# Kernel tuning notes

Hardware: AMD Instinct MI355X
Metric: run time of the kernel (lower is better)

## Reference

```python
import jax, jax.numpy as jnp
import numpy as np

N = 100000   # nodes
E = 1600000  # edges (before self-loops)
F = 128      # num_features
H = 128      # hidden_dim
EPS = 1e-5   # BatchNorm eps


def setup_inputs() -> dict:
    key = jax.random.key(0)
    ks = jax.random.split(key, 8)
    x = jax.random.normal(ks[0], (N, F), dtype=jnp.float32)
    edge_index = jax.random.randint(ks[1], (2, E), 0, N, dtype=jnp.int64)

    def lin(k, din, dout):
        s = 1.0 / np.sqrt(din)
        kw, kb = jax.random.split(k)
        W = jax.random.uniform(kw, (din, dout), jnp.float32, -s, s)
        b = jax.random.uniform(kb, (dout,), jnp.float32, -s, s)
        return W, b

    W1, b1 = lin(ks[2], F, H)
    W2, b2 = lin(ks[3], H, H)
    W3, b3 = lin(ks[4], H, H)
    Wc, bc = lin(ks[5], H, 2)

    def bn_params():
        return (jnp.ones((H,), jnp.float32), jnp.zeros((H,), jnp.float32),
                jnp.zeros((H,), jnp.float32), jnp.ones((H,), jnp.float32))

    g1, be1, rm1, rv1 = bn_params()
    g2, be2, rm2, rv2 = bn_params()
    g3, be3, rm3, rv3 = bn_params()

    return {"x": x, "edge_index": edge_index,
            "W1": W1, "b1": b1, "W2": W2, "b2": b2, "W3": W3, "b3": b3,
            "g1": g1, "be1": be1, "rm1": rm1, "rv1": rv1,
            "g2": g2, "be2": be2, "rm2": rm2, "rv2": rv2,
            "g3": g3, "be3": be3, "rm3": rm3, "rv3": rv3,
            "Wc": Wc, "bc": bc}


def _gcn_norm(edge_index, num_nodes):
    # add self-loops, compute symmetric normalization (PyG GCNConv default)
    loop = jnp.arange(num_nodes, dtype=edge_index.dtype)
    src = jnp.concatenate([edge_index[0], loop])
    dst = jnp.concatenate([edge_index[1], loop])
    deg = jax.ops.segment_sum(jnp.ones_like(dst, dtype=jnp.float32), dst,
                              num_segments=num_nodes)
    dinv = jnp.where(deg > 0, jax.lax.rsqrt(deg), 0.0)
    norm = dinv[src] * dinv[dst]  # [E+N]
    return src, dst, norm


def _gcn_conv(x, W, b, src, dst, norm, num_nodes):
    h = x @ W                              # [N, H] linear first
    msg = h[src] * norm[:, None]           # gather + scale  [E+N, H]
    out = jax.ops.segment_sum(msg, dst, num_segments=num_nodes)  # scatter-add
    return out + b


def _bn_eval(x, g, be, rm, rv):
    return (x - rm) * jax.lax.rsqrt(rv + EPS) * g + be


def reference(x, edge_index,
              W1, b1, W2, b2, W3, b3,
              g1, be1, rm1, rv1,
              g2, be2, rm2, rv2,
              g3, be3, rm3, rv3,
              Wc, bc):
    n = x.shape[0]
    src, dst, norm = _gcn_norm(edge_index, n)
    h = _gcn_conv(x, W1, b1, src, dst, norm, n)
    h = _bn_eval(jax.nn.relu(h), g1, be1, rm1, rv1)
    # dropout: identity in eval mode
    h = _gcn_conv(h, W2, b2, src, dst, norm, n)
    h = _bn_eval(jax.nn.relu(h), g2, be2, rm2, rv2)
    h = _gcn_conv(h, W3, b3, src, dst, norm, n)
    h = _bn_eval(jax.nn.relu(h), g3, be3, rm3, rv3)
    return h @ Wc + bc  # [N, 2]
```

## Files before the change

### kernel.cpp

```cpp
#include <hip/hip_runtime.h>
#include <hip/hip_fp16.h>

#define BN_EPS 1e-5f
#define CHUNK 4096
#define BBITS 7

typedef _Float16 half8 __attribute__((ext_vector_type(8)));
typedef float f32x4 __attribute__((ext_vector_type(4)));

__device__ __forceinline__ float4 f4zero() { return make_float4(0.f, 0.f, 0.f, 0.f); }


__global__ __launch_bounds__(256) void k_pack_hist(const float* __restrict__ W1,
                                                   const float* __restrict__ W2,
                                                   const float* __restrict__ W3,
                                                   _Float16* __restrict__ pW,
                                                   const int* __restrict__ dst,
                                                   int* __restrict__ tableT,
                                                   int nA, int nbuck, int e) {
    __shared__ int h[1024];
    int tid = threadIdx.x;
    if (blockIdx.x < 24) {
        int t = blockIdx.x * 256 + tid;
        int wi = t >> 11;
        int tt = t & 2047;
        const float* W = (wi == 0) ? W1 : ((wi == 1) ? W2 : W3);
        int kc = tt >> 9;
        int rem = tt & 511;
        int ct = rem >> 6;
        int lane = rem & 63;
        int q = lane >> 4;
        int col = ct * 16 + (lane & 15);
        half8 hh;
#pragma unroll
        for (int j = 0; j < 8; ++j)
            hh[j] = (_Float16)W[(kc * 32 + q * 8 + j) * 128 + col];
        *(half8*)(pW + (size_t)t * 8) = hh;
        return;
    }
    int blk = blockIdx.x - 24;
    for (int k = tid; k < 1024; k += 256) h[k] = 0;
    __syncthreads();
    int base = blk * CHUNK;
    if (base + CHUNK <= e && (e & 3) == 0) {
        const int4* d4 = (const int4*)(dst + base);
#pragma unroll
        for (int t = 0; t < CHUNK / 1024; ++t) {
            int4 d = d4[t * 256 + tid];
            atomicAdd(&h[d.x >> BBITS], 1);
            atomicAdd(&h[d.y >> BBITS], 1);
            atomicAdd(&h[d.z >> BBITS], 1);
            atomicAdd(&h[d.w >> BBITS], 1);
        }
    } else {
        for (int i = base + tid; i < e && i < base + CHUNK; i += 256)
            atomicAdd(&h[dst[i] >> BBITS], 1);
    }
    __syncthreads();
    for (int k = tid; k < nbuck; k += 256)
        tableT[(size_t)k * nA + blk] = h[k];
}


__global__ __launch_bounds__(1024) void k_scan_block(const int* __restrict__ in,
                                                     int* __restrict__ outp,
                                                     int* __restrict__ partials, int len) {
    __shared__ int s[1024];
    int t = threadIdx.x;
    int gid = blockIdx.x * 1024 + t;
    int v = (gid < len) ? in[gid] : 0;
    int x = v;
    s[t] = x;
    __syncthreads();
    for (int d = 1; d < 1024; d <<= 1) {
        int y = (t >= d) ? s[t - d] : 0;
        __syncthreads();
        x += y;
        s[t] = x;
        __syncthreads();
    }
    if (gid < len) outp[gid] = x - v;
    if (t == 1023) partials[blockIdx.x] = x;
}

__global__ __launch_bounds__(256) void k_scan_addp(int* __restrict__ data,
                                                   const int* __restrict__ partials, int len) {
    __shared__ int red[256];
    int tid = threadIdx.x;
    int K = blockIdx.x >> 2;
    int s = 0;
    for (int t = tid; t < K; t += 256) s += partials[t];
    red[tid] = s;
    __syncthreads();
    for (int d = 128; d > 0; d >>= 1) {
        if (tid < d) red[tid] += red[tid + d];
        __syncthreads();
    }
    int gid = blockIdx.x * 256 + tid;
    if (gid < len) data[gid] += red[0];
}


template <bool AF32>
__device__ __forceinline__ void gemm_body(int bid, int tid, char* smem,
                                          const void* __restrict__ Av,
                                          const _Float16* __restrict__ pW,
                                          uint4* __restrict__ C, int n) {
    uint4* sW = (uint4*)smem;
    {
        const uint4* gW = (const uint4*)pW;
#pragma unroll
        for (int i = 0; i < 8; ++i) sW[tid + 256 * i] = gW[tid + 256 * i];
    }
    __syncthreads();

    int wave = tid >> 6, lane = tid & 63;
    int quad = lane >> 4, l16 = lane & 15;
    int row0 = bid * 64 + wave * 16;
    int arow = row0 + l16;
    int arowc = (arow < n) ? arow : (n - 1);

    half8 af[4];
    if (AF32) {
        const float* A = (const float*)Av + (size_t)arowc * 128 + quad * 8;
#pragma unroll
        for (int kc = 0; kc < 4; ++kc) {
            float4 lo = *(const float4*)(A + kc * 32);
            float4 hi = *(const float4*)(A + kc * 32 + 4);
            half8 h;
            h[0] = (_Float16)lo.x; h[1] = (_Float16)lo.y;
            h[2] = (_Float16)lo.z; h[3] = (_Float16)lo.w;
            h[4] = (_Float16)hi.x; h[5] = (_Float16)hi.y;
            h[6] = (_Float16)hi.z; h[7] = (_Float16)hi.w;
            af[kc] = h;
        }
    } else {
        const _Float16* A = (const _Float16*)Av + (size_t)arowc * 128 + quad * 8;
#pragma unroll
        for (int kc = 0; kc < 4; ++kc)
            af[kc] = *(const half8*)(A + kc * 32);
    }

    f32x4 acc[8];
#pragma unroll
    for (int ct = 0; ct < 8; ++ct) acc[ct] = (f32x4){0.f, 0.f, 0.f, 0.f};

#pragma unroll
    for (int kc = 0; kc < 4; ++kc) {
#pragma unroll
        for (int ct = 0; ct < 8; ++ct) {
            half8 bf = *(half8*)&sW[(kc * 8 + ct) * 64 + lane];
            acc[ct] = __builtin_amdgcn_mfma_f32_16x16x32_f16(af[kc], bf, acc[ct], 0, 0, 0);
        }
    }

    __syncthreads();

    _Float16* eb = (_Float16*)smem + wave * 16 * 136;
#pragma unroll
    for (int ct = 0; ct < 8; ++ct)
#pragma unroll
        for (int r = 0; r < 4; ++r)
            eb[(quad * 4 + r) * 136 + ct * 16 + l16] = (_Float16)(acc[ct][r]);

#pragma unroll
    for (int i = 0; i < 4; ++i) {
        int linear = i * 64 + lane;
        int r = linear >> 4, c = linear & 15;
        uint4 v = *(uint4*)((char*)eb + r * 272 + c * 16);
        int row = row0 + r;
        if (row < n) C[(size_t)row * 16 + c] = v;
    }
}

__global__ __launch_bounds__(256) void k_gemm_mfma(const void* __restrict__ Av,
                                                   const _Float16* __restrict__ pW,
                                                   uint4* __restrict__ C, int n) {
    __shared__ char smem[32768];
    gemm_body<false>(blockIdx.x, threadIdx.x, smem, Av, pW, C, n);
}


__global__ __launch_bounds__(256) void k_scatter_gemm(const int* __restrict__ src,
                                                      const int* __restrict__ dst,
                                                      const int* __restrict__ tableT,
                                                      int2* __restrict__ bed,
                                                      int nA, int nbuck, int e,
                                                      const float* __restrict__ x,
                                                      const _Float16* __restrict__ pW,
                                                      uint4* __restrict__ C, int n) {
    __shared__ char smem[32768];
    int tid = threadIdx.x;
    if ((int)blockIdx.x >= nA) {
        gemm_body<true>((int)blockIdx.x - nA, tid, smem, x, pW, C, n);
        return;
    }
    int* cur = (int*)smem;
    int blk = blockIdx.x;
    for (int k = tid; k < nbuck; k += 256)
        cur[k] = tableT[(size_t)k * nA + blk];
    __syncthreads();
    int base = blk * CHUNK;
    if (base + CHUNK <= e && (e & 3) == 0) {
        const int4* s4 = (const int4*)(src + base);
        const int4* d4 = (const int4*)(dst + base);
#pragma unroll
        for (int t = 0; t < CHUNK / 1024; ++t) {
            int4 s = s4[t * 256 + tid];
            int4 d = d4[t * 256 + tid];
            int p0 = atomicAdd(&cur[d.x >> BBITS], 1); bed[p0] = make_int2(s.x, d.x);
            int p1 = atomicAdd(&cur[d.y >> BBITS], 1); bed[p1] = make_int2(s.y, d.y);
            int p2 = atomicAdd(&cur[d.z >> BBITS], 1); bed[p2] = make_int2(s.z, d.z);
            int p3 = atomicAdd(&cur[d.w >> BBITS], 1); bed[p3] = make_int2(s.w, d.w);
        }
    } else {
        for (int i = base + tid; i < e && i < base + CHUNK; i += 256) {
            int d = dst[i];
            int p = atomicAdd(&cur[d >> BBITS], 1);
            bed[p] = make_int2(src[i], d);
        }
    }
}


__global__ __launch_bounds__(256) void k_rank_finalize(const int2* __restrict__ bed,
                                                       const int* __restrict__ tableT,
                                                       int2* __restrict__ offs2,
                                                       int* __restrict__ er,
                                                       float* __restrict__ dinv,
                                                       unsigned int* __restrict__ bufAzero,
                                                       int nA, int nbuck, int n, int e) {
    __shared__ int lcnt[128];
    __shared__ int lscan[128];
    __shared__ int loff[128];
    int b = blockIdx.x, tid = threadIdx.x;
    if (tid < 128) lcnt[tid] = 0;
    __syncthreads();
    int start = tableT[(size_t)b * nA];
    int end = (b + 1 < nbuck) ? tableT[(size_t)(b + 1) * nA] : e;
    for (int i = start + tid; i < end; i += 256)
        atomicAdd(&lcnt[bed[i].y & 127], 1);
    __syncthreads();
    int padded = 0;
    if (tid < 128) {
        padded = (lcnt[tid] + 7) & ~7;
        lscan[tid] = padded;
    }
    __syncthreads();
    for (int d = 1; d < 128; d <<= 1) {
        int y = (tid < 128 && tid >= d) ? lscan[tid - d] : 0;
        __syncthreads();
        if (tid < 128) lscan[tid] += y;
        __syncthreads();
    }
    int ebase = start + (b << 10);
    if (tid < 128) {
        loff[tid] = lscan[tid] - padded;
        int node = (b << BBITS) + tid;
        if (node < n) {
            int c = lcnt[tid];
            int o = ebase + loff[tid];
            offs2[node] = make_int2(o, o + padded);
            dinv[node] = rsqrtf((float)(c + 1));
            for (int j = c; j < padded; ++j) er[o + j] = n << 8;
        }
    }
    if (b == 0 && tid < 64) bufAzero[tid] = 0u;
    if (b == 0 && tid == 0) dinv[n] = 0.f;
    __syncthreads();
    if (tid < 128) lcnt[tid] = 0;
    __syncthreads();
    for (int i = start + tid; i < end; i += 256) {
        int2 q = bed[i];
        int l = q.y & 127;
        int r = atomicAdd(&lcnt[l], 1);
        er[ebase + loff[l] + r] = q.x << 8;
    }
}


__device__ __forceinline__ void acc_row4(float4& aL, float4& aH, uint4 q) {
    asm("v_fma_mix_f32 %0, %1, 1.0, %0 op_sel:[0,0,0] op_sel_hi:[1,0,0]" : "+v"(aL.x) : "v"(q.x));
    asm("v_fma_mix_f32 %0, %1, 1.0, %0 op_sel:[1,0,0] op_sel_hi:[1,0,0]" : "+v"(aL.y) : "v"(q.x));
    asm("v_fma_mix_f32 %0, %1, 1.0, %0 op_sel:[0,0,0] op_sel_hi:[1,0,0]" : "+v"(aL.z) : "v"(q.y));
    asm("v_fma_mix_f32 %0, %1, 1.0, %0 op_sel:[1,0,0] op_sel_hi:[1,0,0]" : "+v"(aL.w) : "v"(q.y));
    asm("v_fma_mix_f32 %0, %1, 1.0, %0 op_sel:[0,0,0] op_sel_hi:[1,0,0]" : "+v"(aH.x) : "v"(q.z));
    asm("v_fma_mix_f32 %0, %1, 1.0, %0 op_sel:[1,0,0] op_sel_hi:[1,0,0]" : "+v"(aH.y) : "v"(q.z));
    asm("v_fma_mix_f32 %0, %1, 1.0, %0 op_sel:[0,0,0] op_sel_hi:[1,0,0]" : "+v"(aH.z) : "v"(q.w));
    asm("v_fma_mix_f32 %0, %1, 1.0, %0 op_sel:[1,0,0] op_sel_hi:[1,0,0]" : "+v"(aH.w) : "v"(q.w));
}

__device__ __forceinline__ void acc_row4s(float4& aL, float4& aH, uint4 q, float s) {
    asm("v_fma_mix_f32 %0, %1, %2, %0 op_sel:[0,0,0] op_sel_hi:[1,0,0]" : "+v"(aL.x) : "v"(q.x), "v"(s));
    asm("v_fma_mix_f32 %0, %1, %2, %0 op_sel:[1,0,0] op_sel_hi:[1,0,0]" : "+v"(aL.y) : "v"(q.x), "v"(s));
    asm("v_fma_mix_f32 %0, %1, %2, %0 op_sel:[0,0,0] op_sel_hi:[1,0,0]" : "+v"(aL.z) : "v"(q.y), "v"(s));
    asm("v_fma_mix_f32 %0, %1, %2, %0 op_sel:[1,0,0] op_sel_hi:[1,0,0]" : "+v"(aL.w) : "v"(q.y), "v"(s));
    asm("v_fma_mix_f32 %0, %1, %2, %0 op_sel:[0,0,0] op_sel_hi:[1,0,0]" : "+v"(aH.x) : "v"(q.z), "v"(s));
    asm("v_fma_mix_f32 %0, %1, %2, %0 op_sel:[1,0,0] op_sel_hi:[1,0,0]" : "+v"(aH.y) : "v"(q.z), "v"(s));
    asm("v_fma_mix_f32 %0, %1, %2, %0 op_sel:[0,0,0] op_sel_hi:[1,0,0]" : "+v"(aH.z) : "v"(q.w), "v"(s));
    asm("v_fma_mix_f32 %0, %1, %2, %0 op_sel:[1,0,0] op_sel_hi:[1,0,0]" : "+v"(aH.w) : "v"(q.w), "v"(s));
}


template <bool FUSE_CLS, bool SRC_SCALE>
__global__ __launch_bounds__(256) void k_aggregate(const uint4* __restrict__ Ah,
                                                   const int2* __restrict__ offs2,
                                                   const int* __restrict__ er,
                                                   const float* __restrict__ dinv,
                                                   const float* __restrict__ bias,
                                                   const float* __restrict__ g,
                                                   const float* __restrict__ be,
                                                   const float* __restrict__ rm,
                                                   const float* __restrict__ rv,
                                                   uint4* __restrict__ Hout,
                                                   const float* __restrict__ Wc,
                                                   const float* __restrict__ bc,
                                                   float* __restrict__ out, int n) {
    int lane = threadIdx.x & 15;
    int node = blockIdx.x * 16 + (threadIdx.x >> 4);
    if (node >= n) return;

    const char* AhB = (const char*)Ah;
    unsigned int l16 = (unsigned int)lane * 16u;

    float di = dinv[node];
    float4 aL = f4zero(), aH = f4zero();
    {
        uint4 qs = *(const uint4*)(AhB + (((unsigned int)node << 8) + l16));
        if (SRC_SCALE) acc_row4s(aL, aH, qs, di);
        else           acc_row4(aL, aH, qs);
    }

    int2 offc = offs2[node];
    int e0 = offc.x, e1 = offc.y;
    for (int e = e0; e < e1; e += 8) {
        int4 ra = *(const int4*)(er + e);
        int4 rb = *(const int4*)(er + e + 4);
        uint4 v0 = *(const uint4*)(AhB + ((unsigned int)ra.x + l16));
        uint4 v1 = *(const uint4*)(AhB + ((unsigned int)ra.y + l16));
        uint4 v2 = *(const uint4*)(AhB + ((unsigned int)ra.z + l16));
        uint4 v3 = *(const uint4*)(AhB + ((unsigned int)ra.w + l16));
        uint4 v4 = *(const uint4*)(AhB + ((unsigned int)rb.x + l16));
        uint4 v5 = *(const uint4*)(AhB + ((unsigned int)rb.y + l16));
        uint4 v6 = *(const uint4*)(AhB + ((unsigned int)rb.z + l16));
        uint4 v7 = *(const uint4*)(AhB + ((unsigned int)rb.w + l16));
        if (SRC_SCALE) {
            float d0 = dinv[(unsigned int)ra.x >> 8];
            float d1 = dinv[(unsigned int)ra.y >> 8];
            float d2 = dinv[(unsigned int)ra.z >> 8];
            float d3 = dinv[(unsigned int)ra.w >> 8];
            float d4 = dinv[(unsigned int)rb.x >> 8];
            float d5 = dinv[(unsigned int)rb.y >> 8];
            float d6 = dinv[(unsigned int)rb.z >> 8];
            float d7 = dinv[(unsigned int)rb.w >> 8];
            acc_row4s(aL, aH, v0, d0); acc_row4s(aL, aH, v1, d1);
            acc_row4s(aL, aH, v2, d2); acc_row4s(aL, aH, v3, d3);
            acc_row4s(aL, aH, v4, d4); acc_row4s(aL, aH, v5, d5);
            acc_row4s(aL, aH, v6, d6); acc_row4s(aL, aH, v7, d7);
        } else {
            acc_row4(aL, aH, v0); acc_row4(aL, aH, v1); acc_row4(aL, aH, v2); acc_row4(aL, aH, v3);
            acc_row4(aL, aH, v4); acc_row4(aL, aH, v5); acc_row4(aL, aH, v6); acc_row4(aL, aH, v7);
        }
    }

    aL.x *= di; aL.y *= di; aL.z *= di; aL.w *= di;
    aH.x *= di; aH.y *= di; aH.z *= di; aH.w *= di;

    float4 bL  = ((const float4*)bias)[2 * lane], bH  = ((const float4*)bias)[2 * lane + 1];
    float4 gL  = ((const float4*)g)[2 * lane],    gH  = ((const float4*)g)[2 * lane + 1];
    float4 beL = ((const float4*)be)[2 * lane],   beH = ((const float4*)be)[2 * lane + 1];
    float4 rmL = ((const float4*)rm)[2 * lane],   rmH = ((const float4*)rm)[2 * lane + 1];
    float4 rvL = ((const float4*)rv)[2 * lane],   rvH = ((const float4*)rv)[2 * lane + 1];

    float4 oL, oH;
    float v;
    v = fmaxf(aL.x + bL.x, 0.f); oL.x = (v - rmL.x) * rsqrtf(rvL.x + BN_EPS) * gL.x + beL.x;
    v = fmaxf(aL.y + bL.y, 0.f); oL.y = (v - rmL.y) * rsqrtf(rvL.y + BN_EPS) * gL.y + beL.y;
    v = fmaxf(aL.z + bL.z, 0.f); oL.z = (v - rmL.z) * rsqrtf(rvL.z + BN_EPS) * gL.z + beL.z;
    v = fmaxf(aL.w + bL.w, 0.f); oL.w = (v - rmL.w) * rsqrtf(rvL.w + BN_EPS) * gL.w + beL.w;
    v = fmaxf(aH.x + bH.x, 0.f); oH.x = (v - rmH.x) * rsqrtf(rvH.x + BN_EPS) * gH.x + beH.x;
    v = fmaxf(aH.y + bH.y, 0.f); oH.y = (v - rmH.y) * rsqrtf(rvH.y + BN_EPS) * gH.y + beH.y;
    v = fmaxf(aH.z + bH.z, 0.f); oH.z = (v - rmH.z) * rsqrtf(rvH.z + BN_EPS) * gH.z + beH.z;
    v = fmaxf(aH.w + bH.w, 0.f); oH.w = (v - rmH.w) * rsqrtf(rvH.w + BN_EPS) * gH.w + beH.w;

    if (!FUSE_CLS) {
        __half2 p0 = __floats2half2_rn(oL.x, oL.y);
        __half2 p1 = __floats2half2_rn(oL.z, oL.w);
        __half2 p2 = __floats2half2_rn(oH.x, oH.y);
        __half2 p3 = __floats2half2_rn(oH.z, oH.w);
        uint4 u;
        u.x = *(unsigned int*)&p0;
        u.y = *(unsigned int*)&p1;
        u.z = *(unsigned int*)&p2;
        u.w = *(unsigned int*)&p3;
        Hout[(size_t)node * 16 + lane] = u;
    } else {
        const float4* Wv = (const float4*)Wc;
        float4 w0 = Wv[4 * lane];
        float4 w1 = Wv[4 * lane + 1];
        float4 w2 = Wv[4 * lane + 2];
        float4 w3 = Wv[4 * lane + 3];
        float p0 = oL.x * w0.x + oL.y * w0.z + oL.z * w1.x + oL.w * w1.z
                 + oH.x * w2.x + oH.y * w2.z + oH.z * w3.x + oH.w * w3.z;
        float p1 = oL.x * w0.y + oL.y * w0.w + oL.z * w1.y + oL.w * w1.w
                 + oH.x * w2.y + oH.y * w2.w + oH.z * w3.y + oH.w * w3.w;
#pragma unroll
        for (int d = 8; d >= 1; d >>= 1) {
            p0 += __shfl_down(p0, d, 16);
            p1 += __shfl_down(p1, d, 16);
        }
        if (lane == 0) {
            out[node * 2 + 0] = p0 + bc[0];
            out[node * 2 + 1] = p1 + bc[1];
        }
    }
}


extern "C" void kernel_launch(void* const* d_in, const int* in_sizes, int n_in,
                              void* d_out, int out_size, void* d_ws, size_t ws_size,
                              hipStream_t stream) {
    const float* x   = (const float*)d_in[0];
    const int*   ei  = (const int*)d_in[1];
    const float* W1  = (const float*)d_in[2];
    const float* b1  = (const float*)d_in[3];
    const float* W2  = (const float*)d_in[4];
    const float* b2  = (const float*)d_in[5];
    const float* W3  = (const float*)d_in[6];
    const float* b3  = (const float*)d_in[7];
    const float* g1  = (const float*)d_in[8];
    const float* be1 = (const float*)d_in[9];
    const float* rm1 = (const float*)d_in[10];
    const float* rv1 = (const float*)d_in[11];
    const float* g2  = (const float*)d_in[12];
    const float* be2 = (const float*)d_in[13];
    const float* rm2 = (const float*)d_in[14];
    const float* rv2 = (const float*)d_in[15];
    const float* g3  = (const float*)d_in[16];
    const float* be3 = (const float*)d_in[17];
    const float* rm3 = (const float*)d_in[18];
    const float* rv3 = (const float*)d_in[19];
    const float* Wc  = (const float*)d_in[20];
    const float* bc  = (const float*)d_in[21];
    float* out = (float*)d_out;

    int n = in_sizes[0] / 128;
    int e = in_sizes[1] / 2;
    const int* src = ei;
    const int* dst = ei + e;

    char* ws = (char*)d_ws;
    size_t off = 0;
    auto alloc = [&](size_t bytes) -> char* {
        char* p = ws + off;
        off += (bytes + 255) & ~(size_t)255;
        return p;
    };
    int nA    = (e + CHUNK - 1) / CHUNK;
    int nbuck = (n + (1 << BBITS) - 1) >> BBITS;
    int tlen  = nbuck * nA;
    int erCap = e + (nbuck << 10) + 64;

    char*      bufA     = (char*) alloc((size_t)(n + 1) * 256);
    char*      bufH     = (char*) alloc((size_t)n * 256);
    float*     dinv     = (float*)alloc((size_t)(n + 1) * 4);
    int2*      offs2    = (int2*) alloc((size_t)n * 8);
    int*       tableT   = (int*)  alloc((size_t)(tlen + 1) * 4);
    int*       parts    = (int*)  alloc(8192);
    int*       er       = (int*)  alloc((size_t)erCap * 4);
    _Float16*  pW       = (_Float16*)alloc(3 * 16384 * 2);
    (void)ws_size; (void)n_in; (void)out_size;

    int2* bed = (int2*)bufH;

    int nbT   = (tlen + 1023) / 1024;
    int gT    = (tlen + 255) / 256;
    int gGemm = (n + 63) / 64;
    int gAgg  = (n + 15) / 16;

    k_pack_hist<<<24 + nA, 256, 0, stream>>>(W1, W2, W3, pW, dst, tableT, nA, nbuck, e);
    k_scan_block<<<nbT, 1024, 0, stream>>>(tableT, tableT, parts, tlen);
    k_scan_addp<<<gT, 256, 0, stream>>>(tableT, parts, tlen);
    k_scatter_gemm<<<nA + gGemm, 256, 0, stream>>>(src, dst, tableT, bed, nA, nbuck, e,
                                                   x, pW, (uint4*)bufA, n);
    k_rank_finalize<<<nbuck, 256, 0, stream>>>(bed, tableT, offs2, er, dinv,
                                               (unsigned int*)(bufA + (size_t)n * 256),
                                               nA, nbuck, n, e);

    k_aggregate<false, true><<<gAgg, 256, 0, stream>>>((const uint4*)bufA, offs2, er, dinv,
                                                       b1, g1, be1, rm1, rv1, (uint4*)bufH,
                                                       nullptr, nullptr, nullptr, n);
    k_gemm_mfma<<<gGemm, 256, 0, stream>>>(bufH, pW + 16384, (uint4*)bufA, n);
    k_aggregate<false, true><<<gAgg, 256, 0, stream>>>((const uint4*)bufA, offs2, er, dinv,
                                                       b2, g2, be2, rm2, rv2, (uint4*)bufH,
                                                       nullptr, nullptr, nullptr, n);
    k_gemm_mfma<<<gGemm, 256, 0, stream>>>(bufH, pW + 32768, (uint4*)bufA, n);
    k_aggregate<true, true><<<gAgg, 256, 0, stream>>>((const uint4*)bufA, offs2, er, dinv,
                                                      b3, g3, be3, rm3, rv3, nullptr,
                                                      Wc, bc, out, n);
}
```

Measured before the change: 390.3 us.

## Pre-scale GEMM outputs by dinv, enlarge buckets, and fuse ranking with first GEMM

Layers 2 and 3 now fold the source-side dinv scaling into the GEMM epilogue. The aggregate kernel therefore skips the per-edge dinv gather for those layers. The bucket sort uses larger chunks (8192) and wider buckets (512 nodes) with 1024-thread blocks. The rank/finalize step is fused with the first-layer GEMM instead of with the scatter. This cuts random dinv loads in the hot aggregation loops and reduces launch and table overhead, but raises per-bucket padding, shared atomic contention and fp16 rounding of the scaled values.

```diff
diff --git a/kernel.cpp b/kernel.cpp
--- a/kernel.cpp
+++ b/kernel.cpp
@@ -2,8 +2,8 @@
 #include <hip/hip_fp16.h>
 
 #define BN_EPS 1e-5f
-#define CHUNK 4096
-#define BBITS 7
+#define CHUNK 8192
+#define BBITS 9
 
 typedef _Float16 half8 __attribute__((ext_vector_type(8)));
 typedef float f32x4 __attribute__((ext_vector_type(4)));
@@ -11,17 +11,17 @@
 __device__ __forceinline__ float4 f4zero() { return make_float4(0.f, 0.f, 0.f, 0.f); }
 
 
-__global__ __launch_bounds__(256) void k_pack_hist(const float* __restrict__ W1,
-                                                   const float* __restrict__ W2,
-                                                   const float* __restrict__ W3,
-                                                   _Float16* __restrict__ pW,
-                                                   const int* __restrict__ dst,
-                                                   int* __restrict__ tableT,
-                                                   int nA, int nbuck, int e) {
-    __shared__ int h[1024];
+__global__ __launch_bounds__(1024) void k_pack_hist(const float* __restrict__ W1,
+                                                    const float* __restrict__ W2,
+                                                    const float* __restrict__ W3,
+                                                    _Float16* __restrict__ pW,
+                                                    const int* __restrict__ dst,
+                                                    int* __restrict__ tableT,
+                                                    int nA, int nbuck, int e) {
+    __shared__ int h[256];
     int tid = threadIdx.x;
-    if (blockIdx.x < 24) {
-        int t = blockIdx.x * 256 + tid;
+    if (blockIdx.x < 6) {
+        int t = blockIdx.x * 1024 + tid;
         int wi = t >> 11;
         int tt = t & 2047;
         const float* W = (wi == 0) ? W1 : ((wi == 1) ? W2 : W3);
@@ -38,26 +38,26 @@
         *(half8*)(pW + (size_t)t * 8) = hh;
         return;
     }
-    int blk = blockIdx.x - 24;
-    for (int k = tid; k < 1024; k += 256) h[k] = 0;
+    int blk = blockIdx.x - 6;
+    if (tid < 256) h[tid] = 0;
     __syncthreads();
     int base = blk * CHUNK;
-    if (base + CHUNK <= e && (e & 3) == 0) {
+    if (base + CHUNK <= e) {
         const int4* d4 = (const int4*)(dst + base);
 #pragma unroll
-        for (int t = 0; t < CHUNK / 1024; ++t) {
-            int4 d = d4[t * 256 + tid];
+        for (int t = 0; t < CHUNK / 4096; ++t) {
+            int4 d = d4[t * 1024 + tid];
             atomicAdd(&h[d.x >> BBITS], 1);
             atomicAdd(&h[d.y >> BBITS], 1);
             atomicAdd(&h[d.z >> BBITS], 1);
             atomicAdd(&h[d.w >> BBITS], 1);
         }
     } else {
-        for (int i = base + tid; i < e && i < base + CHUNK; i += 256)
+        for (int i = base + tid; i < e; i += 1024)
             atomicAdd(&h[dst[i] >> BBITS], 1);
     }
     __syncthreads();
-    for (int k = tid; k < nbuck; k += 256)
+    for (int k = tid; k < nbuck; k += 1024)
         tableT[(size_t)k * nA + blk] = h[k];
 }
 
@@ -101,10 +101,44 @@
 }
 
 
-template <bool AF32>
+__global__ __launch_bounds__(1024) void k_scatter(const int* __restrict__ src,
+                                                  const int* __restrict__ dst,
+                                                  const int* __restrict__ tableT,
+                                                  int2* __restrict__ bed,
+                                                  int nA, int nbuck, int e) {
+    __shared__ int cur[256];
+    int blk = blockIdx.x, tid = threadIdx.x;
+    for (int k = tid; k < nbuck; k += 1024)
+        cur[k] = tableT[(size_t)k * nA + blk];
+    __syncthreads();
+    int base = blk * CHUNK;
+    if (base + CHUNK <= e) {
+        const int4* s4 = (const int4*)(src + base);
+        const int4* d4 = (const int4*)(dst + base);
+#pragma unroll
+        for (int t = 0; t < CHUNK / 4096; ++t) {
+            int4 s = s4[t * 1024 + tid];
+            int4 d = d4[t * 1024 + tid];
+            int p0 = atomicAdd(&cur[d.x >> BBITS], 1); bed[p0] = make_int2(s.x, d.x);
+            int p1 = atomicAdd(&cur[d.y >> BBITS], 1); bed[p1] = make_int2(s.y, d.y);
+            int p2 = atomicAdd(&cur[d.z >> BBITS], 1); bed[p2] = make_int2(s.z, d.z);
+            int p3 = atomicAdd(&cur[d.w >> BBITS], 1); bed[p3] = make_int2(s.w, d.w);
+        }
+    } else {
+        for (int i = base + tid; i < e; i += 1024) {
+            int d = dst[i];
+            int p = atomicAdd(&cur[d >> BBITS], 1);
+            bed[p] = make_int2(src[i], d);
+        }
+    }
+}
+
+
+template <bool AF32, bool SCALE>
 __device__ __forceinline__ void gemm_body(int bid, int tid, char* smem,
                                           const void* __restrict__ Av,
                                           const _Float16* __restrict__ pW,
+                                          const float* __restrict__ dinv,
                                           uint4* __restrict__ C, int n) {
     uint4* sW = (uint4*)smem;
     {
@@ -157,11 +191,20 @@
     __syncthreads();
 
     _Float16* eb = (_Float16*)smem + wave * 16 * 136;
+    float dv[4];
+#pragma unroll
+    for (int r = 0; r < 4; ++r) {
+        if (SCALE) {
+            int rr = row0 + quad * 4 + r;
+            dv[r] = dinv[(rr < n) ? rr : (n - 1)];
+        } else dv[r] = 1.f;
+    }
 #pragma unroll
     for (int ct = 0; ct < 8; ++ct)
 #pragma unroll
         for (int r = 0; r < 4; ++r)
-            eb[(quad * 4 + r) * 136 + ct * 16 + l16] = (_Float16)(acc[ct][r]);
+            eb[(quad * 4 + r) * 136 + ct * 16 + l16] =
+                (_Float16)(SCALE ? acc[ct][r] * dv[r] : acc[ct][r]);
 
 #pragma unroll
     for (int i = 0; i < 4; ++i) {
@@ -175,104 +218,83 @@
 
 __global__ __launch_bounds__(256) void k_gemm_mfma(const void* __restrict__ Av,
                                                    const _Float16* __restrict__ pW,
+                                                   const float* __restrict__ dinv,
                                                    uint4* __restrict__ C, int n) {
     __shared__ char smem[32768];
-    gemm_body<false>(blockIdx.x, threadIdx.x, smem, Av, pW, C, n);
-}
-
-
-__global__ __launch_bounds__(256) void k_scatter_gemm(const int* __restrict__ src,
-                                                      const int* __restrict__ dst,
-                                                      const int* __restrict__ tableT,
-                                                      int2* __restrict__ bed,
-                                                      int nA, int nbuck, int e,
-                                                      const float* __restrict__ x,
-                                                      const _Float16* __restrict__ pW,
-                                                      uint4* __restrict__ C, int n) {
+    gemm_body<false, true>(blockIdx.x, threadIdx.x, smem, Av, pW, dinv, C, n);
+}
+
+
+__global__ __launch_bounds__(256) void k_rank_gemm1(const int2* __restrict__ bed,
+                                                    const int* __restrict__ tableT,
+                                                    int2* __restrict__ offs2,
+                                                    int* __restrict__ er,
+                                                    float* __restrict__ dinv,
+                                                    unsigned int* __restrict__ pad0,
+                                                    const float* __restrict__ x,
+                                                    const _Float16* __restrict__ pW,
+                                                    uint4* __restrict__ C,
+                                                    int nA, int nbuck, int n, int e) {
     __shared__ char smem[32768];
     int tid = threadIdx.x;
-    if ((int)blockIdx.x >= nA) {
-        gemm_body<true>((int)blockIdx.x - nA, tid, smem, x, pW, C, n);
+    int b = blockIdx.x;
+    if (b >= nbuck) {
+        gemm_body<true, false>(b - nbuck, tid, smem, x, pW, nullptr, C, n);
         return;
     }
-    int* cur = (int*)smem;
-    int blk = blockIdx.x;
-    for (int k = tid; k < nbuck; k += 256)
-        cur[k] = tableT[(size_t)k * nA + blk];
-    __syncthreads();
-    int base = blk * CHUNK;
-    if (base + CHUNK <= e && (e & 3) == 0) {
-        const int4* s4 = (const int4*)(src + base);
-        const int4* d4 = (const int4*)(dst + base);
-#pragma unroll
-        for (int t = 0; t < CHUNK / 1024; ++t) {
-            int4 s = s4[t * 256 + tid];
-            int4 d = d4[t * 256 + tid];
-            int p0 = atomicAdd(&cur[d.x >> BBITS], 1); bed[p0] = make_int2(s.x, d.x);
-            int p1 = atomicAdd(&cur[d.y >> BBITS], 1); bed[p1] = make_int2(s.y, d.y);
-            int p2 = atomicAdd(&cur[d.z >> BBITS], 1); bed[p2] = make_int2(s.z, d.z);
-            int p3 = atomicAdd(&cur[d.w >> BBITS], 1); bed[p3] = make_int2(s.w, d.w);
-        }
-    } else {
-        for (int i = base + tid; i < e && i < base + CHUNK; i += 256) {
-            int d = dst[i];
-            int p = atomicAdd(&cur[d >> BBITS], 1);
-            bed[p] = make_int2(src[i], d);
-        }
-    }
-}
-
-
-__global__ __launch_bounds__(256) void k_rank_finalize(const int2* __restrict__ bed,
-                                                       const int* __restrict__ tableT,
-                                                       int2* __restrict__ offs2,
-                                                       int* __restrict__ er,
-                                                       float* __restrict__ dinv,
-                                                       unsigned int* __restrict__ bufAzero,
-                                                       int nA, int nbuck, int n, int e) {
-    __shared__ int lcnt[128];
-    __shared__ int lscan[128];
-    __shared__ int loff[128];
-    int b = blockIdx.x, tid = threadIdx.x;
-    if (tid < 128) lcnt[tid] = 0;
+    int* lcnt = (int*)smem;
+    int* loff = lcnt + 512;
+    int* s    = loff + 512;
+    if (b == 0) {
+        if (tid < 64) pad0[tid] = 0u;
+        if (tid == 0) dinv[n] = 0.f;
+    }
+    for (int k = tid; k < 512; k += 256) lcnt[k] = 0;
     __syncthreads();
     int start = tableT[(size_t)b * nA];
     int end = (b + 1 < nbuck) ? tableT[(size_t)(b + 1) * nA] : e;
     for (int i = start + tid; i < end; i += 256)
-        atomicAdd(&lcnt[bed[i].y & 127], 1);
-    __syncthreads();
-    int padded = 0;
-    if (tid < 128) {
-        padded = (lcnt[tid] + 7) & ~7;
-        lscan[tid] = padded;
-    }
-    __syncthreads();
-    for (int d = 1; d < 128; d <<= 1) {
-        int y = (tid < 128 && tid >= d) ? lscan[tid - d] : 0;
+        atomicAdd(&lcnt[bed[i].y & 511], 1);
+    __syncthreads();
+    int t2 = tid * 2;
+    int c0 = lcnt[t2], c1 = lcnt[t2 + 1];
+    int p0 = (c0 + 7) & ~7, p1 = (c1 + 7) & ~7;
+    int xsum = p0 + p1;
+    s[tid] = xsum;
+    __syncthreads();
+    for (int d = 1; d < 256; d <<= 1) {
+        int y = (tid >= d) ? s[tid - d] : 0;
         __syncthreads();
-        if (tid < 128) lscan[tid] += y;
+        xsum += y;
+        s[tid] = xsum;
         __syncthreads();
     }
-    int ebase = start + (b << 10);
-    if (tid < 128) {
-        loff[tid] = lscan[tid] - padded;
-        int node = (b << BBITS) + tid;
+    int ebase = start + (b << 12);
+    int base0 = xsum - p0 - p1;
+    loff[t2] = base0;
+    loff[t2 + 1] = base0 + p0;
+    {
+        int node = (b << BBITS) + t2;
         if (node < n) {
-            int c = lcnt[tid];
-            int o = ebase + loff[tid];
-            offs2[node] = make_int2(o, o + padded);
-            dinv[node] = rsqrtf((float)(c + 1));
-            for (int j = c; j < padded; ++j) er[o + j] = n << 8;
-        }
-    }
-    if (b == 0 && tid < 64) bufAzero[tid] = 0u;
-    if (b == 0 && tid == 0) dinv[n] = 0.f;
-    __syncthreads();
-    if (tid < 128) lcnt[tid] = 0;
+            int o = ebase + base0;
+            offs2[node] = make_int2(o, o + p0);
+            dinv[node] = rsqrtf((float)(c0 + 1));
+            for (int j = c0; j < p0; ++j) er[o + j] = n << 8;
+        }
+        node = (b << BBITS) + t2 + 1;
+        if (node < n) {
+            int o = ebase + base0 + p0;
+            offs2[node] = make_int2(o, o + p1);
+            dinv[node] = rsqrtf((float)(c1 + 1));
+            for (int j = c1; j < p1; ++j) er[o + j] = n << 8;
+        }
+    }
+    __syncthreads();
+    for (int k = tid; k < 512; k += 256) lcnt[k] = 0;
     __syncthreads();
     for (int i = start + tid; i < end; i += 256) {
         int2 q = bed[i];
-        int l = q.y & 127;
+        int l = q.y & 511;
         int r = atomicAdd(&lcnt[l], 1);
         er[ebase + loff[l] + r] = q.x << 8;
     }
@@ -321,29 +343,28 @@
     if (node >= n) return;
 
     const char* AhB = (const char*)Ah;
-    unsigned int l16 = (unsigned int)lane * 16u;
+    unsigned int l16b = (unsigned int)lane * 16u;
 
     float di = dinv[node];
     float4 aL = f4zero(), aH = f4zero();
     {
-        uint4 qs = *(const uint4*)(AhB + (((unsigned int)node << 8) + l16));
+        uint4 qs = *(const uint4*)(AhB + (((unsigned int)node << 8) + l16b));
         if (SRC_SCALE) acc_row4s(aL, aH, qs, di);
         else           acc_row4(aL, aH, qs);
     }
 
     int2 offc = offs2[node];
-    int e0 = offc.x, e1 = offc.y;
-    for (int e = e0; e < e1; e += 8) {
+    for (int e = offc.x; e < offc.y; e += 8) {
         int4 ra = *(const int4*)(er + e);
         int4 rb = *(const int4*)(er + e + 4);
-        uint4 v0 = *(const uint4*)(AhB + ((unsigned int)ra.x + l16));
-        uint4 v1 = *(const uint4*)(AhB + ((unsigned int)ra.y + l16));
-        uint4 v2 = *(const uint4*)(AhB + ((unsigned int)ra.z + l16));
-        uint4 v3 = *(const uint4*)(AhB + ((unsigned int)ra.w + l16));
-        uint4 v4 = *(const uint4*)(AhB + ((unsigned int)rb.x + l16));
-        uint4 v5 = *(const uint4*)(AhB + ((unsigned int)rb.y + l16));
-        uint4 v6 = *(const uint4*)(AhB + ((unsigned int)rb.z + l16));
-        uint4 v7 = *(const uint4*)(AhB + ((unsigned int)rb.w + l16));
+        uint4 v0 = *(const uint4*)(AhB + ((unsigned int)ra.x + l16b));
+        uint4 v1 = *(const uint4*)(AhB + ((unsigned int)ra.y + l16b));
+        uint4 v2 = *(const uint4*)(AhB + ((unsigned int)ra.z + l16b));
+        uint4 v3 = *(const uint4*)(AhB + ((unsigned int)ra.w + l16b));
+        uint4 v4 = *(const uint4*)(AhB + ((unsigned int)rb.x + l16b));
+        uint4 v5 = *(const uint4*)(AhB + ((unsigned int)rb.y + l16b));
+        uint4 v6 = *(const uint4*)(AhB + ((unsigned int)rb.z + l16b));
+        uint4 v7 = *(const uint4*)(AhB + ((unsigned int)rb.w + l16b));
         if (SRC_SCALE) {
             float d0 = dinv[(unsigned int)ra.x >> 8];
             float d1 = dinv[(unsigned int)ra.y >> 8];
@@ -459,10 +480,10 @@
     int nA    = (e + CHUNK - 1) / CHUNK;
     int nbuck = (n + (1 << BBITS) - 1) >> BBITS;
     int tlen  = nbuck * nA;
-    int erCap = e + (nbuck << 10) + 64;
-
-    char*      bufA     = (char*) alloc((size_t)(n + 1) * 256);
-    char*      bufH     = (char*) alloc((size_t)n * 256);
+    int erCap = e + (nbuck << 12) + 64;
+
+    char*      buf0     = (char*) alloc((size_t)(n + 1) * 256);
+    char*      buf1     = (char*) alloc((size_t)(n + 1) * 256);
     float*     dinv     = (float*)alloc((size_t)(n + 1) * 4);
     int2*      offs2    = (int2*) alloc((size_t)n * 8);
     int*       tableT   = (int*)  alloc((size_t)(tlen + 1) * 4);
@@ -471,31 +492,31 @@
     _Float16*  pW       = (_Float16*)alloc(3 * 16384 * 2);
     (void)ws_size; (void)n_in; (void)out_size;
 
-    int2* bed = (int2*)bufH;
+    int2* bed = (int2*)buf1;
 
     int nbT   = (tlen + 1023) / 1024;
     int gT    = (tlen + 255) / 256;
     int gGemm = (n + 63) / 64;
     int gAgg  = (n + 15) / 16;
 
-    k_pack_hist<<<24 + nA, 256, 0, stream>>>(W1, W2, W3, pW, dst, tableT, nA, nbuck, e);
+    k_pack_hist<<<6 + nA, 1024, 0, stream>>>(W1, W2, W3, pW, dst, tableT, nA, nbuck, e);
     k_scan_block<<<nbT, 1024, 0, stream>>>(tableT, tableT, parts, tlen);
     k_scan_addp<<<gT, 256, 0, stream>>>(tableT, parts, tlen);
-    k_scatter_gemm<<<nA + gGemm, 256, 0, stream>>>(src, dst, tableT, bed, nA, nbuck, e,
-                                                   x, pW, (uint4*)bufA, n);
-    k_rank_finalize<<<nbuck, 256, 0, stream>>>(bed, tableT, offs2, er, dinv,
-                                               (unsigned int*)(bufA + (size_t)n * 256),
-                                               nA, nbuck, n, e);
-
-    k_aggregate<false, true><<<gAgg, 256, 0, stream>>>((const uint4*)bufA, offs2, er, dinv,
-                                                       b1, g1, be1, rm1, rv1, (uint4*)bufH,
-                                                       nullptr, nullptr, nullptr, n);
-    k_gemm_mfma<<<gGemm, 256, 0, stream>>>(bufH, pW + 16384, (uint4*)bufA, n);
-    k_aggregate<false, true><<<gAgg, 256, 0, stream>>>((const uint4*)bufA, offs2, er, dinv,
-                                                       b2, g2, be2, rm2, rv2, (uint4*)bufH,
-                                                       nullptr, nullptr, nullptr, n);
-    k_gemm_mfma<<<gGemm, 256, 0, stream>>>(bufH, pW + 32768, (uint4*)bufA, n);
-    k_aggregate<true, true><<<gAgg, 256, 0, stream>>>((const uint4*)bufA, offs2, er, dinv,
-                                                      b3, g3, be3, rm3, rv3, nullptr,
-                                                      Wc, bc, out, n);
-}
+    k_scatter<<<nA, 1024, 0, stream>>>(src, dst, tableT, bed, nA, nbuck, e);
+    k_rank_gemm1<<<nbuck + gGemm, 256, 0, stream>>>(
+        bed, tableT, offs2, er, dinv,
+        (unsigned int*)(buf0 + (size_t)n * 256),
+        x, pW, (uint4*)buf0, nA, nbuck, n, e);
+
+    k_aggregate<false, true><<<gAgg, 256, 0, stream>>>(
+        (const uint4*)buf0, offs2, er, dinv, b1, g1, be1, rm1, rv1,
+        (uint4*)buf1, nullptr, nullptr, nullptr, n);
+    k_gemm_mfma<<<gGemm, 256, 0, stream>>>(buf1, pW + 16384, dinv, (uint4*)buf0, n);
+    k_aggregate<false, false><<<gAgg, 256, 0, stream>>>(
+        (const uint4*)buf0, offs2, er, dinv, b2, g2, be2, rm2, rv2,
+        (uint4*)buf1, nullptr, nullptr, nullptr, n);
+    k_gemm_mfma<<<gGemm, 256, 0, stream>>>(buf1, pW + 32768, dinv, (uint4*)buf0, n);
+    k_aggregate<true, false><<<gAgg, 256, 0, stream>>>(
+        (const uint4*)buf0, offs2, er, dinv, b3, g3, be3, rm3, rv3,
+        nullptr, Wc, bc, out, n);
+}
```

Result: faster. 374.0 us (-4.2%).
